# Performance work log

Hardware: AMD Instinct MI355X
Metric: run time of the kernel (lower is better)

Reference implementation:

```python
import jax, jax.numpy as jnp
import numpy as np
from jax import lax

B, T, IDIM, HDIM = 128, 256, 64, 128
TS, KS, OC1, ANF = 64, 3, 100, 64
S1 = TS - 3 * (KS - 1)   # 58: three VALID ks=3 stride-1 convs
S = S1 * S1              # 3364
HN = 2 * HDIM            # 256 = h_dim * l_dim (l_dim=2)
F = S + HN               # 3620
HID = F // 2             # 1810


def _conv(x, w, b):
    y = lax.conv_general_dilated(x, w, (1, 1), 'VALID',
                                 dimension_numbers=('NCHW', 'OIHW', 'NCHW'))
    return y + b[None, :, None, None]


def _lstm_layer(x, w_ih, w_hh, b_ih, b_hh):
    # x: [B, T, D] -> (outputs [B, T, H], final hidden [B, H]); PyTorch gate order i,f,g,o
    Bn = x.shape[0]
    h0 = jnp.zeros((Bn, HDIM), x.dtype)
    c0 = jnp.zeros((Bn, HDIM), x.dtype)
    def step(carry, xt):
        h, c = carry
        g = xt @ w_ih.T + h @ w_hh.T + b_ih + b_hh
        i, f, gg, o = jnp.split(g, 4, axis=-1)
        c = jax.nn.sigmoid(f) * c + jax.nn.sigmoid(i) * jnp.tanh(gg)
        h = jax.nn.sigmoid(o) * jnp.tanh(c)
        return (h, c), h
    (hT, cT), ys = lax.scan(step, (h0, c0), jnp.swapaxes(x, 0, 1))
    return jnp.swapaxes(ys, 0, 1), hT


def setup_inputs() -> dict:
    key = jax.random.key(0)
    k = jax.random.split(key, 30)
    s = 0.05
    H4 = 4 * HDIM
    return {
        'x1': jax.random.normal(k[0], (B, 3, TS, TS), jnp.float32),
        'x2': jax.random.normal(k[1], (B, T, IDIM), jnp.float32),
        # conv2a/conv2b: two Monte-Carlo weight samples of the same Bayesian conv2 layer
        'conv1_w': jax.random.normal(k[2], (OC1, 3, KS, KS), jnp.float32) * s,
        'conv1_b': jax.random.normal(k[3], (OC1,), jnp.float32) * s,
        'conv2a_w': jax.random.normal(k[4], (OC1, OC1, KS, KS), jnp.float32) * s,
        'conv2a_b': jax.random.normal(k[5], (OC1,), jnp.float32) * s,
        'conv2b_w': jax.random.normal(k[6], (OC1, OC1, KS, KS), jnp.float32) * s,
        'conv2b_b': jax.random.normal(k[7], (OC1,), jnp.float32) * s,
        'w_ih0': jax.random.normal(k[8], (H4, IDIM), jnp.float32) * s,
        'w_hh0': jax.random.normal(k[9], (H4, HDIM), jnp.float32) * s,
        'b_ih0': jax.random.normal(k[10], (H4,), jnp.float32) * s,
        'b_hh0': jax.random.normal(k[11], (H4,), jnp.float32) * s,
        'w_ih1': jax.random.normal(k[12], (H4, HDIM), jnp.float32) * s,
        'w_hh1': jax.random.normal(k[13], (H4, HDIM), jnp.float32) * s,
        'b_ih1': jax.random.normal(k[14], (H4,), jnp.float32) * s,
        'b_hh1': jax.random.normal(k[15], (H4,), jnp.float32) * s,
        'attn1_w': jax.random.normal(k[16], (ANF, F), jnp.float32) * s,
        'attn1_b': jax.random.normal(k[17], (ANF,), jnp.float32) * s,
        'attn2_w': jax.random.normal(k[18], (1, ANF), jnp.float32) * s,
        'attn2_b': jax.random.normal(k[19], (1,), jnp.float32) * s,
        'fc1_w': jax.random.normal(k[20], (HID, F), jnp.float32) * s,
        'fc1_b': jax.random.normal(k[21], (HID,), jnp.float32) * s,
        'fc2_w': jax.random.normal(k[22], (1, HID), jnp.float32) * s,
        'fc2_b': jax.random.normal(k[23], (1,), jnp.float32) * s,
    }


def reference(x1, x2, conv1_w, conv1_b, conv2a_w, conv2a_b, conv2b_w, conv2b_b,
              w_ih0, w_hh0, b_ih0, b_hh0, w_ih1, w_hh1, b_ih1, b_hh1,
              attn1_w, attn1_b, attn2_w, attn2_b, fc1_w, fc1_b, fc2_w, fc2_b):
    Bn = x1.shape[0]
    # CNN branch
    x = jax.nn.relu(_conv(x1, conv1_w, conv1_b))
    x = jax.nn.relu(_conv(x, conv2a_w, conv2a_b))
    x = jax.nn.relu(_conv(x, conv2b_w, conv2b_b))
    xd = x.reshape(Bn, OC1, S)                               # [B, oc1, S]
    # LSTM branch (2 layers, dropout in eval mode = identity)
    y0, h0f = _lstm_layer(x2, w_ih0, w_hh0, b_ih0, b_hh0)
    _, h1f = _lstm_layer(y0, w_ih1, w_hh1, b_ih1, b_hh1)
    hn = jnp.concatenate([h0f, h1f], axis=1)                 # [B, 2*h_dim]
    # Broadcast hidden state across channels (replaces the torch concat loop)
    hn_b = jnp.broadcast_to(hn[:, None, :], (Bn, OC1, HN))
    fused = jnp.concatenate([xd, hn_b], axis=2)              # [B, oc1, F]
    # Attention
    a = jnp.tanh(fused @ attn1_w.T + attn1_b)                # [B, oc1, anf]
    a = a @ attn2_w.T + attn2_b                              # [B, oc1, 1]
    a = jax.nn.softmax(a, axis=1)
    ctx = jnp.einsum('bcs,bco->bso', xd, a).reshape(Bn, S)   # [B, S]
    # Fusion MLP (dropout eval-mode identity)
    m = jnp.concatenate([ctx, hn], axis=1)                   # [B, F]
    h = jax.nn.relu(m @ fc1_w.T + fc1_b)
    return h @ fc2_w.T + fc2_b                               # [B, 1]
```

## Files before the change

kernel.cpp:

```cpp
#include <hip/hip_runtime.h>
#include <hip/hip_bf16.h>
#include <math.h>

#define BB 128
#define TT 256
#define IDIM 64
#define HD 128
#define G4 512
#define OC 100
#define W1 62
#define W2 60
#define W3 58
#define NPX1 (W1*W1)
#define NPX2 (W2*W2)
#define NPX3 (W3*W3)
#define SS NPX3
#define FF (SS + 2*HD)
#define HIDN 1810
#define ANF 64

typedef __hip_bfloat16 bf16;
typedef _Float16 f16;
typedef __attribute__((ext_vector_type(8))) short bf16x8;
typedef __attribute__((ext_vector_type(4))) short bf16x4;
typedef __attribute__((ext_vector_type(2))) _Float16 half2v;
typedef __attribute__((ext_vector_type(4))) float f32x4;

__device__ __forceinline__ float ldf(const float* p) { return *p; }
__device__ __forceinline__ float ldf(const bf16* p)  { return __bfloat162float(*p); }
__device__ __forceinline__ void  stf(float* p, float v) { *p = v; }
__device__ __forceinline__ void  stf(bf16* p, float v)  { *p = __float2bfloat16(v); }

__device__ __forceinline__ short f2bs(float v) {
    bf16 t = __float2bfloat16(v); short s; __builtin_memcpy(&s, &t, 2); return s;
}
__device__ __forceinline__ float fsig(float x) {
    return __builtin_amdgcn_rcpf(1.f + __expf(-x));
}
__device__ __forceinline__ float ftanh(float x) {
    float t = __expf(-2.f * fabsf(x));
    float r = __builtin_amdgcn_rcpf(1.f + t);
    float m = 1.f - 2.f * t * r;
    return copysignf(m, x);
}
__device__ __forceinline__ float fmix2(unsigned w, unsigned h, float acc) {
    half2v wv, hv;
    __builtin_memcpy(&wv, &w, 4);
    __builtin_memcpy(&hv, &h, 4);
    acc = fmaf((float)wv[0], (float)hv[0], acc);
    acc = fmaf((float)wv[1], (float)hv[1], acc);
    return acc;
}

__device__ __forceinline__ bf16x8 load8(const bf16* p) { return *(const bf16x8*)p; }
__device__ __forceinline__ bf16x8 load8(const float* p) {
    float4 x = *(const float4*)p;
    float4 y = *(const float4*)(p + 4);
    bf16x8 r;
    r[0] = f2bs(x.x); r[1] = f2bs(x.y); r[2] = f2bs(x.z); r[3] = f2bs(x.w);
    r[4] = f2bs(y.x); r[5] = f2bs(y.y); r[6] = f2bs(y.z); r[7] = f2bs(y.w);
    return r;
}

__global__ void zero_kernel(float* o, int n)
{
    int i = blockIdx.x * 256 + threadIdx.x;
    if (i < n) o[i] = 0.f;
}

__device__ __forceinline__ void body_cvt_bf16(const float* __restrict__ s, bf16* __restrict__ d,
                                              int i, int n4)
{
    if (i >= n4) return;
    float4 v = ((const float4*)s)[i];
    bf16x4 o;
    o[0] = f2bs(v.x); o[1] = f2bs(v.y); o[2] = f2bs(v.z); o[3] = f2bs(v.w);
    *(bf16x4*)(d + 4 * (size_t)i) = o;
}
__device__ __forceinline__ void body_cvt_f16(const float* __restrict__ s, f16* __restrict__ d,
                                             int i, int n4)
{
    if (i >= n4) return;
    float4 v = ((const float4*)s)[i];
    f16 o[4] = {(f16)v.x, (f16)v.y, (f16)v.z, (f16)v.w};
    *(uint2*)(d + 4 * (size_t)i) = *(uint2*)o;
}
__device__ __forceinline__ void body_wt(const float* __restrict__ w, bf16* __restrict__ WT, int idx)
{
    if (idx >= 129024) return;
    int i  = idx & 31;
    int oc = (idx >> 5) % 112;
    int ts = idx / (112 * 32);
    int s = ts & 3, t = ts >> 2;
    int ic = s * 32 + i;
    float v = 0.f;
    if (oc < OC && ic < OC) v = w[(oc * OC + ic) * 9 + t];
    WT[idx] = __float2bfloat16(v);
}

__global__ __launch_bounds__(256)
void prep_kernel(const float* __restrict__ x2,   bf16* __restrict__ X2B,
                 const float* __restrict__ whh0, f16*  __restrict__ LWf0,
                 const float* __restrict__ whh1, f16*  __restrict__ LWf1,
                 const float* __restrict__ wih0, bf16* __restrict__ WIH0B,
                 const float* __restrict__ wih1, bf16* __restrict__ WIH1B,
                 const float* __restrict__ a1w,  bf16* __restrict__ A1WB,
                 const float* __restrict__ bih0, const float* __restrict__ bhh0, float* __restrict__ BS0,
                 const float* __restrict__ bih1, const float* __restrict__ bhh1, float* __restrict__ BS1,
                 const float* __restrict__ c2aw, bf16* __restrict__ WTa,
                 const float* __restrict__ c2bw, bf16* __restrict__ WTb)
{
    int bid = blockIdx.x;
    int tid = threadIdx.x;
    if (bid < 2048)      body_cvt_bf16(x2,   X2B,   bid * 256 + tid, 524288);
    else if (bid < 2112) body_cvt_f16 (whh0, LWf0, (bid - 2048) * 256 + tid, 16384);
    else if (bid < 2176) body_cvt_f16 (whh1, LWf1, (bid - 2112) * 256 + tid, 16384);
    else if (bid < 2208) body_cvt_bf16(wih0, WIH0B, (bid - 2176) * 256 + tid, 8192);
    else if (bid < 2272) body_cvt_bf16(wih1, WIH1B, (bid - 2208) * 256 + tid, 16384);
    else if (bid < 2499) body_cvt_bf16(a1w,  A1WB,  (bid - 2272) * 256 + tid, 57920);
    else if (bid < 2500) { BS0[tid] = bih0[tid] + bhh0[tid]; BS0[tid + 256] = bih0[tid + 256] + bhh0[tid + 256]; }
    else if (bid < 2501) { BS1[tid] = bih1[tid] + bhh1[tid]; BS1[tid + 256] = bih1[tid + 256] + bhh1[tid + 256]; }
    else if (bid < 3005) body_wt(c2aw, WTa, (bid - 2501) * 256 + tid);
    else                 body_wt(c2bw, WTb, (bid - 3005) * 256 + tid);
}

__device__ __forceinline__
void conv1_body(const float* __restrict__ x1, const float* __restrict__ wl,
                const float* __restrict__ bl, bf16* __restrict__ out, int b, int py, int t)
{
    int px = py * 256 + t;
    if (px >= NPX1) return;
    int y = px / W1, x = px % W1;
    float in[3][3][3];
    const float* xb = x1 + (size_t)b * 3 * 64 * 64;
#pragma unroll
    for (int ic = 0; ic < 3; ic++)
#pragma unroll
        for (int r = 0; r < 3; r++)
#pragma unroll
            for (int c = 0; c < 3; c++)
                in[ic][r][c] = xb[(ic * 64 + y + r) * 64 + x + c];
    bf16* ob = out + (size_t)b * OC * NPX1 + px;
    for (int oc = 0; oc < OC; ++oc) {
        float acc = bl[oc];
        const float* wp = &wl[oc * 27];
#pragma unroll
        for (int ic = 0; ic < 3; ic++)
#pragma unroll
            for (int r = 0; r < 3; r++)
#pragma unroll
                for (int c = 0; c < 3; c++)
                    acc = fmaf(in[ic][r][c], wp[ic * 9 + r * 3 + c], acc);
        ob[(size_t)oc * NPX1] = __float2bfloat16(fmaxf(acc, 0.f));
    }
}

__global__ __launch_bounds__(256)
void conv1_kernel(const float* __restrict__ x1, const float* __restrict__ w,
                  const float* __restrict__ bias, bf16* __restrict__ out)
{
    __shared__ float wl[2700];
    __shared__ float bl[OC];
    int tid = threadIdx.x;
    for (int i = tid; i < 2700; i += 256) wl[i] = w[i];
    if (tid < OC) bl[tid] = bias[tid];
    __syncthreads();
    conv1_body(x1, wl, bl, out, blockIdx.x, blockIdx.y, tid);
}

__device__ __forceinline__
void conv2_body(const bf16* __restrict__ in, const bf16* __restrict__ WT,
                const float* __restrict__ bias, bf16* __restrict__ out,
                int iw, int ow, int b, int yblk, int tid,
                bf16* __restrict__ il, bf16* __restrict__ wl)
{
    int y0 = yblk * 8;
    int wid = tid >> 6;
    int l = tid & 63;
    int hq = l >> 4;
    int l16 = l & 15;
    int yo = y0 + wid;

    f32x4 acc[7][4];
#pragma unroll
    for (int f = 0; f < 7; f++) {
#pragma unroll
        for (int r = 0; r < 4; r++) {
            int oc = f * 16 + hq * 4 + r;
            float bv = (oc < OC) ? bias[oc] : 0.f;
#pragma unroll
            for (int n = 0; n < 4; n++) acc[f][n][r] = bv;
        }
    }

    const size_t ims = (size_t)iw * iw;
    int icl = tid & 31;
    int t2  = tid >> 5;
    for (int s = 0; s < 4; ++s) {
        __syncthreads();
        int ic = s * 32 + icl;
        bool icok = ic < OC;
        const bf16* ibase = in + (size_t)(b * OC + ic) * ims;
#pragma unroll
        for (int it = 0; it < 6; ++it) {
            int u2 = t2 + it * 16;
            if (u2 < 90) {
                int r = u2 / 9, xb = u2 - r * 9;
                int x8 = xb * 8;
                int yy = y0 + r;
                bf16x8 v = {0, 0, 0, 0, 0, 0, 0, 0};
                if (icok && yy < iw && x8 < iw) {
                    const short* sp = (const short*)(ibase + (size_t)yy * iw + x8);
                    if (x8 + 8 <= iw) {
                        const unsigned* sp32 = (const unsigned*)sp;
#pragma unroll
                        for (int q = 0; q < 4; q++)
                            ((unsigned*)&v)[q] = sp32[q];
                    } else {
                        for (int k = 0; k < 8; k++)
                            if (x8 + k < iw) ((short*)&v)[k] = sp[k];
                    }
                }
                bf16* dst = &il[(r * 72 + x8) * 40 + icl];
#pragma unroll
                for (int k = 0; k < 8; k++)
                    *(short*)&dst[k * 40] = ((short*)&v)[k];
            }
        }
#pragma unroll
        for (int it = 0; it < 8; ++it) {
            int u = tid + it * 512;
            if (u < 4032) {
                int tf = u >> 6; int lp = u & 63;
                int t = tf / 7, f = tf - t * 7;
                int oc = f * 16 + (lp & 15);
                int hq2 = lp >> 4;
                *(bf16x8*)&wl[(size_t)u * 8] =
                    *(const bf16x8*)(WT + (size_t)((t * 4 + s) * 112 + oc) * 32 + hq2 * 8);
            }
        }
        __syncthreads();

#pragma unroll
        for (int ky = 0; ky < 3; ++ky) {
#pragma unroll
            for (int kx = 0; kx < 3; ++kx) {
                int t = ky * 3 + kx;
                bf16x8 a[7];
#pragma unroll
                for (int f = 0; f < 7; f++)
                    a[f] = *(const bf16x8*)&wl[(size_t)((t * 7 + f) * 64 + l) * 8];
                bf16x8 bfr[4];
#pragma unroll
                for (int n = 0; n < 4; n++)
                    bfr[n] = *(const bf16x8*)&il[((wid + ky) * 72 + kx + l16 + n * 16) * 40 + hq * 8];
#pragma unroll
                for (int f = 0; f < 7; f++)
#pragma unroll
                    for (int n = 0; n < 4; n++)
                        acc[f][n] = __builtin_amdgcn_mfma_f32_16x16x32_bf16(
                            a[f], bfr[n], acc[f][n], 0, 0, 0);
            }
        }
    }

    if (yo < ow) {
#pragma unroll
        for (int f = 0; f < 7; f++) {
#pragma unroll
            for (int r = 0; r < 4; r++) {
                int oc = f * 16 + hq * 4 + r;
                if (oc < OC) {
#pragma unroll
                    for (int n = 0; n < 4; n++) {
                        int x = n * 16 + l16;
                        if (x < ow)
                            out[((size_t)(b * OC + oc) * ow + yo) * ow + x] =
                                __float2bfloat16(fmaxf(acc[f][n][r], 0.f));
                    }
                }
            }
        }
    }
}

__global__ __launch_bounds__(512, 1)
void conv2_mfma(const bf16* __restrict__ in, const bf16* __restrict__ WT,
                const float* __restrict__ bias, bf16* __restrict__ out,
                int iw, int ow)
{
    __shared__ bf16 il[10 * 72 * 40];
    __shared__ bf16 wl[4032 * 8];
    conv2_body(in, WT, bias, out, iw, ow, blockIdx.x, blockIdx.y, threadIdx.x, il, wl);
}

__device__ __forceinline__
void lstm_body(const bf16* __restrict__ G, const f16* __restrict__ LWr,
               bf16* __restrict__ Y, float* __restrict__ HN, int hoff,
               int b, int g, f16* __restrict__ hl, float* __restrict__ ex)
{
    uint4 wv[16];
    const uint4* wp = (const uint4*)(LWr + (size_t)g * HD);
#pragma unroll
    for (int q = 0; q < 16; q++) wv[q] = wp[q];
#pragma unroll
    for (int q = 0; q < 16; q++)
        asm volatile("" : "+v"(wv[q].x), "+v"(wv[q].y), "+v"(wv[q].z), "+v"(wv[q].w));
    float c = 0.f;
    if (g < HD) hl[g] = (f16)0.f;
    __syncthreads();
    const bf16* Gb = G + (size_t)b * TT * G4 + g;
    float gcur = __bfloat162float(Gb[0]);
    for (int t = 0; t < TT; ++t) {
        int tn = (t + 1 < TT) ? t + 1 : t;
        bf16 gnext = Gb[(size_t)tn * G4];
        float a0 = 0.f, a1 = 0.f, a2 = 0.f, a3 = 0.f;
#pragma unroll
        for (int q = 0; q < 16; q++) {
            uint4 hw = *(const uint4*)&hl[q * 8];
            a0 = fmix2(wv[q].x, hw.x, a0);
            a1 = fmix2(wv[q].y, hw.y, a1);
            a2 = fmix2(wv[q].z, hw.z, a2);
            a3 = fmix2(wv[q].w, hw.w, a3);
        }
        float dot = gcur + (a0 + a1) + (a2 + a3);
        float tr;
        if (g < 2 * HD || g >= 3 * HD) tr = fsig(dot);
        else tr = ftanh(dot);
        ex[g] = tr;
        gcur = __bfloat162float(gnext);
        __syncthreads();
        if (g < HD) {
            float iv = ex[g], fv = ex[HD + g], gv = ex[2 * HD + g], ov = ex[3 * HD + g];
            c = fv * c + iv * gv;
            float nh = ov * ftanh(c);
            hl[g] = (f16)nh;
            if (Y) Y[((size_t)b * TT + t) * HD + g] = __float2bfloat16(nh);
            if (t == TT - 1) HN[(size_t)b * 256 + hoff + g] = nh;
        }
        __syncthreads();
    }
}

__global__ __launch_bounds__(512, 1)
void lstm_recur(const bf16* __restrict__ G, const f16* __restrict__ LWr,
                bf16* __restrict__ Y, float* __restrict__ HN, int hoff)
{
    __shared__ __align__(16) f16 hl[HD];
    __shared__ float ex[G4];
    lstm_body(G, LWr, Y, HN, hoff, blockIdx.x, threadIdx.x, hl, ex);
}

__global__ __launch_bounds__(512, 1)
void hybrid_l0c1(const bf16* __restrict__ G, const f16* __restrict__ LWf0,
                 bf16* __restrict__ Y0, float* __restrict__ HN,
                 const float* __restrict__ x1, const float* __restrict__ c1w,
                 const float* __restrict__ c1b, bf16* __restrict__ A1)
{
    __shared__ __align__(16) char smem[11264];
    int bid = blockIdx.x;
    if (bid < BB) {
        lstm_body(G, LWf0, Y0, HN, 0, bid, threadIdx.x,
                  (f16*)smem, (float*)(smem + 512));
    } else {
        float* wl = (float*)smem;
        float* bl = (float*)(smem + 10800);
        int tid = threadIdx.x;
        for (int i = tid; i < 2700; i += 512) wl[i] = c1w[i];
        if (tid < OC) bl[tid] = c1b[tid];
        __syncthreads();
        int v = (bid - BB) * 2 + (tid >> 8);
        conv1_body(x1, wl, bl, A1, v >> 4, v & 15, tid & 255);
    }
}

template<typename TB, typename TC, int ACT>
__global__ __launch_bounds__(256)
void gemm_mfma(const bf16* __restrict__ A, int lda,
               const TB* __restrict__ B, int ldb,
               const float* __restrict__ bias,
               TC* __restrict__ C, int ldc,
               int M, int N, int K)
{
    __shared__ bf16 As[64 * 72];
    __shared__ bf16 Bs[64 * 72];
    int tid = threadIdx.x;
    int l = tid & 63, wid = tid >> 6;
    int l16 = l & 15, h = l >> 4;
    int m0 = blockIdx.x * 64, n0 = blockIdx.y * 64;
    f32x4 acc[4];
#pragma unroll
    for (int nb = 0; nb < 4; nb++) acc[nb] = (f32x4){0.f, 0.f, 0.f, 0.f};

    int rs = tid >> 3;
    int kc = (tid & 7) * 8;

    for (int k0 = 0; k0 < K; k0 += 64) {
        int kr = K - k0;
#pragma unroll
        for (int half = 0; half < 2; half++) {
            int rr = rs + half * 32;
            bf16x8 av = {0, 0, 0, 0, 0, 0, 0, 0};
            int m = m0 + rr;
            if (m < M) {
                const short* src = (const short*)(A + (size_t)m * lda + k0 + kc);
                if (kc + 8 <= kr) av = *(const bf16x8*)src;
                else if (kc < kr) {
                    for (int j = 0; j < 8; j++) if (kc + j < kr) ((short*)&av)[j] = src[j];
                }
            }
            *(bf16x8*)&As[rr * 72 + kc] = av;
            bf16x8 bv = {0, 0, 0, 0, 0, 0, 0, 0};
            int n = n0 + rr;
            if (n < N) {
                const TB* src = B + (size_t)n * ldb + k0 + kc;
                if (kc + 8 <= kr) bv = load8(src);
                else if (kc < kr) {
                    for (int j = 0; j < 8; j++) if (kc + j < kr) ((short*)&bv)[j] = f2bs(ldf(src + j));
                }
            }
            *(bf16x8*)&Bs[rr * 72 + kc] = bv;
        }
        __syncthreads();
#pragma unroll
        for (int kk = 0; kk < 2; kk++) {
            bf16x8 af = *(const bf16x8*)&As[(wid * 16 + l16) * 72 + kk * 32 + h * 8];
#pragma unroll
            for (int nb = 0; nb < 4; nb++) {
                bf16x8 bfr = *(const bf16x8*)&Bs[(nb * 16 + l16) * 72 + kk * 32 + h * 8];
                acc[nb] = __builtin_amdgcn_mfma_f32_16x16x32_bf16(af, bfr, acc[nb], 0, 0, 0);
            }
        }
        __syncthreads();
    }
#pragma unroll
    for (int nb = 0; nb < 4; nb++) {
        int col = n0 + nb * 16 + l16;
        if (col >= N) continue;
        float bv = bias ? bias[col] : 0.f;
#pragma unroll
        for (int reg = 0; reg < 4; reg++) {
            int row = m0 + wid * 16 + h * 4 + reg;
            if (row < M) {
                float v = acc[nb][reg] + bv;
                if (ACT == 1) v = fmaxf(v, 0.f);
                stf(&C[(size_t)row * ldc + col], v);
            }
        }
    }
}

template<typename TA, typename TC, int BM, int BN, int BK, int TM, int TN, int ACT>
__global__ __launch_bounds__((BM / TM) * (BN / TN))
void gemm_tn(const TA* __restrict__ A, int lda,
             const float* __restrict__ Bmat, int ldb,
             const float* __restrict__ bias,
             TC* __restrict__ C, int ldc,
             int M, int N, int K)
{
    constexpr int TX = BN / TN;
    constexpr int TY = BM / TM;
    constexpr int NT = TX * TY;
    __shared__ float As[BK][BM + 1];
    __shared__ float Bs[BK][BN + 1];
    int tid = threadIdx.x;
    int tx = tid % TX, ty = tid / TX;
    int m0 = blockIdx.x * BM, n0 = blockIdx.y * BN;
    float acc[TM][TN] = {};
    for (int k0 = 0; k0 < K; k0 += BK) {
        for (int idx = tid; idx < BM * BK; idx += NT) {
            int i = idx / BK, j = idx % BK;
            int m = m0 + i, k = k0 + j;
            As[j][i] = (m < M && k < K) ? ldf(&A[(size_t)m * lda + k]) : 0.f;
        }
        for (int idx = tid; idx < BN * BK; idx += NT) {
            int i = idx / BK, j = idx % BK;
            int n = n0 + i, k = k0 + j;
            Bs[j][i] = (n < N && k < K) ? Bmat[(size_t)n * ldb + k] : 0.f;
        }
        __syncthreads();
#pragma unroll
        for (int k = 0; k < BK; ++k) {
            float av[TM], bv[TN];
#pragma unroll
            for (int i = 0; i < TM; i++) av[i] = As[k][ty * TM + i];
#pragma unroll
            for (int j = 0; j < TN; j++) bv[j] = Bs[k][tx * TN + j];
#pragma unroll
            for (int i = 0; i < TM; i++)
#pragma unroll
                for (int j = 0; j < TN; j++)
                    acc[i][j] += av[i] * bv[j];
        }
        __syncthreads();
    }
#pragma unroll
    for (int i = 0; i < TM; i++) {
        int m = m0 + ty * TM + i;
        if (m >= M) continue;
#pragma unroll
        for (int j = 0; j < TN; j++) {
            int n = n0 + tx * TN + j;
            if (n >= N) continue;
            float v = acc[i][j] + (bias ? bias[n] : 0.f);
            if (ACT == 1) v = fmaxf(v, 0.f);
            stf(&C[(size_t)m * ldc + n], v);
        }
    }
}

__global__ __launch_bounds__(128)
void attn_softmax(const float* __restrict__ T1,
                  const float* __restrict__ HB,
                  const float* __restrict__ a2w,
                  const float* __restrict__ a2b,
                  float* __restrict__ ATT)
{
    __shared__ float hbl[ANF];
    __shared__ float awl[ANF];
    __shared__ float red[128];
    int b = blockIdx.x, tid = threadIdx.x;
    if (tid < ANF) { hbl[tid] = HB[b * ANF + tid]; awl[tid] = a2w[tid]; }
    __syncthreads();
    float lg = -1e30f;
    if (tid < OC) {
        const float* tp = T1 + (size_t)(b * OC + tid) * ANF;
        float s = 0.f;
#pragma unroll 4
        for (int j = 0; j < ANF; j++) s += ftanh(tp[j] + hbl[j]) * awl[j];
        lg = s + a2b[0];
    }
    red[tid] = lg; __syncthreads();
    for (int st = 64; st > 0; st >>= 1) { if (tid < st) red[tid] = fmaxf(red[tid], red[tid + st]); __syncthreads(); }
    float mx = red[0]; __syncthreads();
    float e = (tid < OC) ? __expf(lg - mx) : 0.f;
    red[tid] = e; __syncthreads();
    for (int st = 64; st > 0; st >>= 1) { if (tid < st) red[tid] += red[tid + st]; __syncthreads(); }
    if (tid < OC) ATT[b * OC + tid] = e / red[0];
}

__global__ __launch_bounds__(256)
void ctx_concat(const bf16* __restrict__ XD,
                const float* __restrict__ ATT,
                const float* __restrict__ HN,
                bf16* __restrict__ M)
{
    __shared__ float al[OC];
    int b = blockIdx.x;
    int tid = threadIdx.x;
    if (tid < OC) al[tid] = ATT[b * OC + tid];
    __syncthreads();
    int s = blockIdx.y * 256 + tid;
    if (s < SS) {
        const bf16* xp = XD + (size_t)b * OC * SS + s;
        float acc = 0.f;
#pragma unroll 4
        for (int c = 0; c < OC; c++) acc = fmaf(__bfloat162float(xp[(size_t)c * SS]), al[c], acc);
        M[(size_t)b * FF + s] = __float2bfloat16(acc);
    } else if (s < FF) {
        M[(size_t)b * FF + s] = __float2bfloat16(HN[b * 256 + (s - SS)]);
    }
}

__global__ __launch_bounds__(256)
void fc2_kernel(const float* __restrict__ H1, const float* __restrict__ w,
                const float* __restrict__ bias, float* __restrict__ out)
{
    int tid = threadIdx.x;
    int lane = tid & 63, wid = tid >> 6;
    int b = blockIdx.x * 4 + wid;
    float acc = 0.f;
    for (int j = lane; j < HIDN; j += 64) acc = fmaf(H1[(size_t)b * HIDN + j], w[j], acc);
#pragma unroll
    for (int off = 32; off > 0; off >>= 1) acc += __shfl_down(acc, off, 64);
    if (lane == 0) out[b] = acc + bias[0];
}

extern "C" void kernel_launch(void* const* d_in, const int* in_sizes, int n_in,
                              void* d_out, int out_size, void* d_ws, size_t ws_size,
                              hipStream_t stream)
{
    const float* x1   = (const float*)d_in[0];
    const float* x2   = (const float*)d_in[1];
    const float* c1w  = (const float*)d_in[2];
    const float* c1b  = (const float*)d_in[3];
    const float* c2aw = (const float*)d_in[4];
    const float* c2ab = (const float*)d_in[5];
    const float* c2bw = (const float*)d_in[6];
    const float* c2bb = (const float*)d_in[7];
    const float* wih0 = (const float*)d_in[8];
    const float* whh0 = (const float*)d_in[9];
    const float* bih0 = (const float*)d_in[10];
    const float* bhh0 = (const float*)d_in[11];
    const float* wih1 = (const float*)d_in[12];
    const float* whh1 = (const float*)d_in[13];
    const float* bih1 = (const float*)d_in[14];
    const float* bhh1 = (const float*)d_in[15];
    const float* a1w  = (const float*)d_in[16];
    const float* a1b  = (const float*)d_in[17];
    const float* a2w  = (const float*)d_in[18];
    const float* a2b  = (const float*)d_in[19];
    const float* f1w  = (const float*)d_in[20];
    const float* f1b  = (const float*)d_in[21];
    const float* f2w  = (const float*)d_in[22];
    const float* f2b  = (const float*)d_in[23];
    float* out = (float*)d_out;

    char* base = (char*)d_ws;
    bf16* G0    = (bf16*)(base + 0);
    bf16* Y0    = (bf16*)(base + 33554432);
    bf16* G1    = G0;
    bf16* X2B   = (bf16*)(base + 41943040);
    bf16* WIH0B = (bf16*)(base + 46137344);
    bf16* WIH1B = (bf16*)(base + 46202880);
    f16*  LWf0  = (f16*)(base + 46333952);
    f16*  LWf1  = (f16*)(base + 46465024);
    const size_t LSTM_END = 46596096;

    int nb = 0; size_t ov = 0;
    for (int cand = BB; cand >= 32; cand >>= 1) {
        size_t cnn = (size_t)cand * OC * (NPX1 + NPX2) * 2;
        size_t o = cnn > LSTM_END ? cnn : LSTM_END;
        size_t q = o + 2048 + 2048 + 131072 + 32768
                 + (size_t)cand * OC * 64 * 4
                 + (((size_t)cand * OC * 4 + 255) & ~(size_t)255)
                 + 926720 + 926720 + 258048 + 258048 + 463360;
        if (ws_size >= q) { nb = cand; ov = o; break; }
    }
    if (nb == 0) {
        zero_kernel<<<1, 128, 0, stream>>>(out, out_size);
        return;
    }
    bf16* A1c;
    bf16* A2c;
    if (nb == BB) {
        A2c = (bf16*)(base + 0);
        A1c = (bf16*)(base + (size_t)BB * OC * NPX2 * 2);
    } else {
        A1c = (bf16*)(base + 0);
        A2c = (bf16*)(base + (size_t)nb * OC * NPX1 * 2);
    }
    bf16* XDc = A1c;
    size_t p = ov;
    float* BS0  = (float*)(base + p); p += 2048;
    float* BS1  = (float*)(base + p); p += 2048;
    float* HN   = (float*)(base + p); p += 131072;
    float* HB   = (float*)(base + p); p += 32768;
    float* T1c  = (float*)(base + p); p += (size_t)nb * OC * 64 * 4;
    float* ATTc = (float*)(base + p); p += ((size_t)nb * OC * 4 + 255) & ~(size_t)255;
    bf16*  MBb  = (bf16*)(base + p); p += 926720;
    float* H1   = (float*)(base + p); p += 926720;
    bf16* WTa   = (bf16*)(base + p); p += 258048;
    bf16* WTb   = (bf16*)(base + p); p += 258048;
    bf16* A1WB  = (bf16*)(base + p); p += 463360;

    prep_kernel<<<3509, 256, 0, stream>>>(
        x2, X2B, whh0, LWf0, whh1, LWf1, wih0, WIH0B, wih1, WIH1B, a1w, A1WB,
        bih0, bhh0, BS0, bih1, bhh1, BS1, c2aw, WTa, c2bw, WTb);

    gemm_mfma<bf16, bf16, 0><<<dim3(512, 8), 256, 0, stream>>>(
        X2B, IDIM, WIH0B, IDIM, BS0, G0, G4, BB * TT, G4, IDIM);

    if (nb == BB) {
        hybrid_l0c1<<<BB + BB * 8, 512, 0, stream>>>(
            G0, LWf0, Y0, HN, x1, c1w, c1b, A1c);
        gemm_mfma<bf16, bf16, 0><<<dim3(512, 8), 256, 0, stream>>>(
            Y0, HD, WIH1B, HD, BS1, G1, G4, BB * TT, G4, HD);
        lstm_recur<<<BB, 512, 0, stream>>>(G1, LWf1, (bf16*)nullptr, HN, HD);
        conv2_mfma<<<dim3(BB, 8), 512, 0, stream>>>(A1c, WTa, c2ab, A2c, W1, W2);
        conv2_mfma<<<dim3(BB, 8), 512, 0, stream>>>(A2c, WTb, c2bb, XDc, W2, W3);
        gemm_tn<float, float, 32, 32, 16, 2, 2, 0><<<dim3(4, 2), 256, 0, stream>>>(
            HN, 256, a1w + SS, FF, a1b, HB, ANF, BB, ANF, 256);
        gemm_mfma<bf16, float, 0><<<dim3(BB * OC / 64, 1), 256, 0, stream>>>(
            XDc, SS, A1WB, FF, nullptr, T1c, ANF, BB * OC, ANF, SS);
        attn_softmax<<<BB, 128, 0, stream>>>(T1c, HB, a2w, a2b, ATTc);
        ctx_concat<<<dim3(BB, 15), 256, 0, stream>>>(XDc, ATTc, HN, MBb);
    } else {
        lstm_recur<<<BB, 512, 0, stream>>>(G0, LWf0, Y0, HN, 0);
        gemm_mfma<bf16, bf16, 0><<<dim3(512, 8), 256, 0, stream>>>(
            Y0, HD, WIH1B, HD, BS1, G1, G4, BB * TT, G4, HD);
        lstm_recur<<<BB, 512, 0, stream>>>(G1, LWf1, (bf16*)nullptr, HN, HD);
        gemm_tn<float, float, 32, 32, 16, 2, 2, 0><<<dim3(4, 2), 256, 0, stream>>>(
            HN, 256, a1w + SS, FF, a1b, HB, ANF, BB, ANF, 256);
        for (int c0 = 0; c0 < BB; c0 += nb) {
            conv1_kernel<<<dim3(nb, 16), 256, 0, stream>>>(
                x1 + (size_t)c0 * 3 * 64 * 64, c1w, c1b, A1c);
            conv2_mfma<<<dim3(nb, 8), 512, 0, stream>>>(A1c, WTa, c2ab, A2c, W1, W2);
            conv2_mfma<<<dim3(nb, 8), 512, 0, stream>>>(A2c, WTb, c2bb, XDc, W2, W3);
            gemm_mfma<bf16, float, 0><<<dim3(nb * OC / 64, 1), 256, 0, stream>>>(
                XDc, SS, A1WB, FF, nullptr, T1c, ANF, nb * OC, ANF, SS);
            attn_softmax<<<nb, 128, 0, stream>>>(T1c, HB + (size_t)c0 * ANF, a2w, a2b, ATTc);
            ctx_concat<<<dim3(nb, 15), 256, 0, stream>>>(
                XDc, ATTc, HN + (size_t)c0 * 256, MBb + (size_t)c0 * FF);
        }
    }

    gemm_mfma<float, float, 1><<<dim3(2, 29), 256, 0, stream>>>(
        MBb, FF, f1w, FF, f1b, H1, HIDN, BB, HIDN, FF);
    fc2_kernel<<<BB / 4, 256, 0, stream>>>(H1, f2w, f2b, out);
}
```

Baseline: 1.098 ms.

## Overlap layer-1 LSTM recurrence with part of first conv2 in hybrid kernel

Adds a hybrid kernel whose first 128 blocks run the layer-1 LSTM recurrence while the remaining blocks run the first conv2 on batch rows 47 and up. The rest of conv2a runs afterwards in a separate launch through a new row-offset parameter. The aim is to fill the GPU's idle compute units during the latency-bound sequential LSTM, as was already done for layer 0 with conv1. The LSTM weight buffers move past the conv region in the workspace so they do not overlap activations written concurrently. The split point is hand-tuned, and the large shared-memory allocation in the hybrid kernel limits occupancy for the LSTM blocks.

```diff
diff --git a/kernel.cpp b/kernel.cpp
--- a/kernel.cpp
+++ b/kernel.cpp
@@ -18,6 +18,7 @@
 #define FF (SS + 2*HD)
 #define HIDN 1810
 #define ANF 64
+#define ROWSPLIT 47
 
 typedef __hip_bfloat16 bf16;
 typedef _Float16 f16;
@@ -287,11 +288,11 @@
 __global__ __launch_bounds__(512, 1)
 void conv2_mfma(const bf16* __restrict__ in, const bf16* __restrict__ WT,
                 const float* __restrict__ bias, bf16* __restrict__ out,
-                int iw, int ow)
+                int iw, int ow, int brow0)
 {
     __shared__ bf16 il[10 * 72 * 40];
     __shared__ bf16 wl[4032 * 8];
-    conv2_body(in, WT, bias, out, iw, ow, blockIdx.x, blockIdx.y, threadIdx.x, il, wl);
+    conv2_body(in, WT, bias, out, iw, ow, brow0 + blockIdx.x, blockIdx.y, threadIdx.x, il, wl);
 }
 
 __device__ __forceinline__
@@ -371,6 +372,24 @@
         __syncthreads();
         int v = (bid - BB) * 2 + (tid >> 8);
         conv1_body(x1, wl, bl, A1, v >> 4, v & 15, tid & 255);
+    }
+}
+
+__global__ __launch_bounds__(512, 1)
+void hybrid_l1c2a(const bf16* __restrict__ G, const f16* __restrict__ LWf1,
+                  float* __restrict__ HN,
+                  const bf16* __restrict__ A1, const bf16* __restrict__ WTa,
+                  const float* __restrict__ c2ab, bf16* __restrict__ A2)
+{
+    __shared__ __align__(16) char smem[122112];
+    int bid = blockIdx.x;
+    if (bid < BB) {
+        lstm_body(G, LWf1, (bf16*)nullptr, HN, HD, bid, threadIdx.x,
+                  (f16*)smem, (float*)(smem + 512));
+    } else {
+        int r = bid - BB;
+        conv2_body(A1, WTa, c2ab, A2, W1, W2, ROWSPLIT + (r >> 3), r & 7,
+                   threadIdx.x, (bf16*)smem, (bf16*)(smem + 57600));
     }
 }
 
@@ -613,9 +632,7 @@
     bf16* X2B   = (bf16*)(base + 41943040);
     bf16* WIH0B = (bf16*)(base + 46137344);
     bf16* WIH1B = (bf16*)(base + 46202880);
-    f16*  LWf0  = (f16*)(base + 46333952);
-    f16*  LWf1  = (f16*)(base + 46465024);
-    const size_t LSTM_END = 46596096;
+    const size_t LSTM_END = 46333952;
 
     int nb = 0; size_t ov = 0;
     for (int cand = BB; cand >= 32; cand >>= 1) {
@@ -624,7 +641,8 @@
         size_t q = o + 2048 + 2048 + 131072 + 32768
                  + (size_t)cand * OC * 64 * 4
                  + (((size_t)cand * OC * 4 + 255) & ~(size_t)255)
-                 + 926720 + 926720 + 258048 + 258048 + 463360;
+                 + 926720 + 926720 + 258048 + 258048 + 463360
+                 + 262144;
         if (ws_size >= q) { nb = cand; ov = o; break; }
     }
     if (nb == 0) {
@@ -653,6 +671,8 @@
     bf16* WTa   = (bf16*)(base + p); p += 258048;
     bf16* WTb   = (bf16*)(base + p); p += 258048;
     bf16* A1WB  = (bf16*)(base + p); p += 463360;
+    f16*  LWf0  = (f16*)(base + p); p += 131072;
+    f16*  LWf1  = (f16*)(base + p); p += 131072;
 
     prep_kernel<<<3509, 256, 0, stream>>>(
         x2, X2B, whh0, LWf0, whh1, LWf1, wih0, WIH0B, wih1, WIH1B, a1w, A1WB,
@@ -666,9 +686,10 @@
             G0, LWf0, Y0, HN, x1, c1w, c1b, A1c);
         gemm_mfma<bf16, bf16, 0><<<dim3(512, 8), 256, 0, stream>>>(
             Y0, HD, WIH1B, HD, BS1, G1, G4, BB * TT, G4, HD);
-        lstm_recur<<<BB, 512, 0, stream>>>(G1, LWf1, (bf16*)nullptr, HN, HD);
-        conv2_mfma<<<dim3(BB, 8), 512, 0, stream>>>(A1c, WTa, c2ab, A2c, W1, W2);
-        conv2_mfma<<<dim3(BB, 8), 512, 0, stream>>>(A2c, WTb, c2bb, XDc, W2, W3);
+        hybrid_l1c2a<<<BB + (BB - ROWSPLIT) * 8, 512, 0, stream>>>(
+            G1, LWf1, HN, A1c, WTa, c2ab, A2c);
+        conv2_mfma<<<dim3(ROWSPLIT, 8), 512, 0, stream>>>(A1c, WTa, c2ab, A2c, W1, W2, 0);
+        conv2_mfma<<<dim3(BB, 8), 512, 0, stream>>>(A2c, WTb, c2bb, XDc, W2, W3, 0);
         gemm_tn<float, float, 32, 32, 16, 2, 2, 0><<<dim3(4, 2), 256, 0, stream>>>(
             HN, 256, a1w + SS, FF, a1b, HB, ANF, BB, ANF, 256);
         gemm_mfma<bf16, float, 0><<<dim3(BB * OC / 64, 1), 256, 0, stream>>>(
@@ -685,8 +706,8 @@
         for (int c0 = 0; c0 < BB; c0 += nb) {
             conv1_kernel<<<dim3(nb, 16), 256, 0, stream>>>(
                 x1 + (size_t)c0 * 3 * 64 * 64, c1w, c1b, A1c);
-            conv2_mfma<<<dim3(nb, 8), 512, 0, stream>>>(A1c, WTa, c2ab, A2c, W1, W2);
-            conv2_mfma<<<dim3(nb, 8), 512, 0, stream>>>(A2c, WTb, c2bb, XDc, W2, W3);
+            conv2_mfma<<<dim3(nb, 8), 512, 0, stream>>>(A1c, WTa, c2ab, A2c, W1, W2, 0);
+            conv2_mfma<<<dim3(nb, 8), 512, 0, stream>>>(A2c, WTb, c2bb, XDc, W2, W3, 0);
             gemm_mfma<bf16, float, 0><<<dim3(nb * OC / 64, 1), 256, 0, stream>>>(
                 XDc, SS, A1WB, FF, nullptr, T1c, ANF, nb * OC, ANF, SS);
             attn_softmax<<<nb, 128, 0, stream>>>(T1c, HB + (size_t)c0 * ANF, a2w, a2b, ATTc);
```

New measurement: 1.058 ms (median of 2 runs). 1.04x faster.
